# Performance work log

Measured on AMD Instinct MI355X. Metric: run time of the kernel, lower is better.

Reference implementation:

```python
import jax, jax.numpy as jnp
import numpy as np

B, S, D, E, K = 2, 2048, 1024, 8, 2
H = 4 * D  # FFN hidden


def setup_inputs() -> dict:
    key = jax.random.key(0)
    ks = jax.random.split(key, 6)
    x = jax.random.normal(ks[0], (B, S, D), dtype=jnp.float32)
    # xavier-uniform gate
    lim_g = np.sqrt(6.0 / (D + E)).astype(np.float32)
    W_gate = jax.random.uniform(ks[1], (D, E), minval=-lim_g, maxval=lim_g, dtype=jnp.float32)
    # per-expert FFN params, stacked on leading expert axis
    lim1 = np.sqrt(1.0 / D).astype(np.float32)
    lim2 = np.sqrt(1.0 / H).astype(np.float32)
    W1 = jax.random.uniform(ks[2], (E, D, H), minval=-lim1, maxval=lim1, dtype=jnp.float32)
    b1 = jax.random.uniform(ks[3], (E, H), minval=-lim1, maxval=lim1, dtype=jnp.float32)
    W2 = jax.random.uniform(ks[4], (E, H, D), minval=-lim2, maxval=lim2, dtype=jnp.float32)
    b2 = jax.random.uniform(ks[5], (E, D), minval=-lim2, maxval=lim2, dtype=jnp.float32)
    return {"x": x, "W_gate": W_gate, "W1": W1, "b1": b1, "W2": W2, "b2": b2}


def reference(x, W_gate, W1, b1, W2, b2):
    # gating: topk mask then softmax over kept logits
    gate = jnp.einsum('bsd,de->bse', x, W_gate)                      # [B,S,E]
    kth = jax.lax.top_k(gate, K)[0][..., -1:]                        # k-th largest [B,S,1]
    mask = jax.nn.softmax(jnp.where(gate >= kth, gate, -jnp.inf), axis=-1)
    # all-experts FFN (faithful to original dense compute)
    h = jax.nn.relu(jnp.einsum('bsd,edh->bseh', x, W1) + b1)         # [B,S,E,H]
    y = jnp.einsum('bseh,ehd->bsed', h, W2) + b2                     # [B,S,E,D]
    # masked MEAN over experts (original uses .mean, i.e. divides by E)
    return (y * mask[..., None]).mean(axis=-2)                       # [B,S,D]
```

## Files before the change

kernel.cpp:

```cpp
#include <hip/hip_runtime.h>
#include <stdint.h>
#include <stddef.h>

#define TOK   4096
#define DDIM  1024
#define EXP   8
#define HDIM  4096

typedef __bf16 bf16x8 __attribute__((ext_vector_type(8)));
typedef __bf16 bf16x4 __attribute__((ext_vector_type(4)));
typedef __bf16 bf16x2 __attribute__((ext_vector_type(2)));
typedef float  f32x4  __attribute__((ext_vector_type(4)));

#define OFF_COUNTS 0ull
#define OFF_PREFIX 256ull
#define OFF_PERM   512ull
#define OFF_WGT    (OFF_PERM + 131072ull)
#define OFF_XBF    (OFF_WGT + 131072ull)
#define OFF_W1T    (OFF_XBF + 8388608ull)
#define OFF_W2T    (OFF_W1T + 67108864ull)
#define OFF_HBF    (OFF_W2T + 67108864ull)
#define OFF_T2E    (OFF_HBF + 68157440ull)

__device__ __forceinline__ void load16_lds(const void* g, void* l) {
  __builtin_amdgcn_global_load_lds((__attribute__((address_space(1))) void*)g,
                                   (__attribute__((address_space(3))) void*)l,
                                   16, 0, 0);
}

__global__ __launch_bounds__(256) void prep_kernel(
    const float* __restrict__ W1, const float* __restrict__ W2,
    __bf16* __restrict__ W1t, __bf16* __restrict__ W2t,
    const float* __restrict__ x, const float* __restrict__ Wg,
    __bf16* __restrict__ x_bf, int* __restrict__ counts,
    int* __restrict__ perm, float* __restrict__ wgt,
    int4* __restrict__ tok2exp)
{
  __shared__ __align__(16) float tile[2112];
  const int bid = blockIdx.x;
  const int tid = threadIdx.x;

  if (bid < 64) {
    const int lane = tid & 63;
    const int wid  = tid >> 6;

    int*   lcnt   = (int*)tile;
    int*   gbase  = lcnt + 8;
    int*   rec_e  = gbase + 8;
    int*   rec_p  = rec_e + 64;
    float* rec_w0 = (float*)(rec_p + 64);
    float* rec_w1 = rec_w0 + 64;

    if (tid < 8) lcnt[tid] = 0;
    __syncthreads();

#pragma unroll 1
    for (int i = 0; i < 16; ++i) {
      const int li = wid * 16 + i;
      const int t  = bid * 64 + li;
      const float* xr = x + (size_t)t * DDIM;

      float acc[EXP];
#pragma unroll
      for (int e = 0; e < EXP; ++e) acc[e] = 0.f;

#pragma unroll
      for (int it = 0; it < 4; ++it) {
        const int d0 = it * 256 + lane * 4;
        float4 xv = *(const float4*)(xr + d0);
        bf16x4 xb = { (__bf16)xv.x, (__bf16)xv.y, (__bf16)xv.z, (__bf16)xv.w };
        *(bf16x4*)(x_bf + (size_t)t * DDIM + d0) = xb;
        const float* wrow = Wg + (size_t)d0 * EXP;
        float xs[4] = { xv.x, xv.y, xv.z, xv.w };
#pragma unroll
        for (int u = 0; u < 4; ++u) {
          float4 wa = *(const float4*)(wrow + u * 8);
          float4 wb = *(const float4*)(wrow + u * 8 + 4);
          acc[0] += xs[u] * wa.x; acc[1] += xs[u] * wa.y;
          acc[2] += xs[u] * wa.z; acc[3] += xs[u] * wa.w;
          acc[4] += xs[u] * wb.x; acc[5] += xs[u] * wb.y;
          acc[6] += xs[u] * wb.z; acc[7] += xs[u] * wb.w;
        }
      }
#pragma unroll
      for (int e = 0; e < EXP; ++e) {
        float v = acc[e];
#pragma unroll
        for (int s = 32; s > 0; s >>= 1) v += __shfl_down(v, s, 64);
        acc[e] = v;
      }
      if (lane == 0) {
        int e0 = 0; float g0 = acc[0];
#pragma unroll
        for (int e = 1; e < EXP; ++e) if (acc[e] > g0) { g0 = acc[e]; e0 = e; }
        int e1 = 0; float g1 = -3.4e38f;
#pragma unroll
        for (int e = 0; e < EXP; ++e) if (e != e0 && acc[e] > g1) { g1 = acc[e]; e1 = e; }
        float ex = __expf(g1 - g0);
        float m0 = 1.f / (1.f + ex);
        float m1 = ex  / (1.f + ex);
        int lp0 = atomicAdd(&lcnt[e0], 1);
        int lp1 = atomicAdd(&lcnt[e1], 1);
        rec_e[li]  = e0 | (e1 << 8);
        rec_p[li]  = lp0 | (lp1 << 16);
        rec_w0[li] = m0 * 0.125f;
        rec_w1[li] = m1 * 0.125f;
      }
    }
    __syncthreads();
    if (tid < 8) gbase[tid] = atomicAdd(&counts[tid], lcnt[tid]);
    __syncthreads();
    if (tid < 64) {
      const int t = bid * 64 + tid;
      const int ee = rec_e[tid], pp = rec_p[tid];
      const int e0 = ee & 0xff, e1 = ee >> 8;
      const int p0 = gbase[e0] + (pp & 0xffff);
      const int p1 = gbase[e1] + (pp >> 16);
      perm[e0 * TOK + p0] = t;  wgt[e0 * TOK + p0] = rec_w0[tid];
      perm[e1 * TOK + p1] = t;  wgt[e1 * TOK + p1] = rec_w1[tid];
      tok2exp[t] = make_int4(e0, p0, e1, p1);
    }
    return;
  }

  const int tb    = bid - 64;
  const int which = tb >> 13;
  const int e     = (tb >> 10) & 7;
  const int t10   = tb & 1023;
  const float* src; __bf16* dst; int Kd, Nd, tk, tn;
  if (which == 0) { Kd = 1024; Nd = 4096; src = W1; dst = W1t; tk = t10 & 15; tn = t10 >> 4; }
  else            { Kd = 4096; Nd = 1024; src = W2; dst = W2t; tk = t10 >> 4; tn = t10 & 15; }
  const int k0 = tk * 64, n0 = tn * 64;
  src += ((size_t)e * Kd + k0) * Nd + n0;
  dst += ((size_t)e * Nd + n0) * Kd + k0;

  char* tb8 = (char*)tile;
  const int lr2 = (tid >> 4) * 2;
  const int lc  = (tid & 15) * 4;
#pragma unroll
  for (int p = 0; p < 2; ++p) {
    const int r = p * 32 + lr2;
    float4 va = *(const float4*)(src + (size_t)r * Nd + lc);
    float4 vb = *(const float4*)(src + (size_t)(r + 1) * Nd + lc);
    float a4[4] = { va.x, va.y, va.z, va.w };
    float b4[4] = { vb.x, vb.y, vb.z, vb.w };
#pragma unroll
    for (int j = 0; j < 4; ++j) {
      const int n = lc + j;
      bf16x2 w = { (__bf16)a4[j], (__bf16)b4[j] };
      *(bf16x2*)(tb8 + n * 128 + ((r * 2) ^ (((n >> 2) & 7) << 4))) = w;
    }
  }
  __syncthreads();
  const int n2 = tid >> 2, cb = tid & 3;
  const int sw = (n2 >> 2) & 7;
#pragma unroll
  for (int h = 0; h < 2; ++h) {
    const int c = cb + h * 4;
    bf16x8 o = *(const bf16x8*)(tb8 + n2 * 128 + ((c ^ sw) << 4));
    *(bf16x8*)(dst + (size_t)n2 * Kd + c * 8) = o;
  }
}

__global__ __launch_bounds__(256, 2) void gemm1_kernel(
    const __bf16* __restrict__ x_bf, const __bf16* __restrict__ W1t,
    const float* __restrict__ b1, __bf16* __restrict__ h_bf,
    const int* __restrict__ perm, const int* __restrict__ counts)
{
  const int bid = blockIdx.x;
  const int e   = bid >> 10;
  const int mt  = (bid >> 5) & 31;
  const int nt  = bid & 31;
  const int cnt = counts[e];
  if (mt * 128 >= cnt) return;
  int pfx = 0;
#pragma unroll
  for (int i = 0; i < EXP; ++i) if (i < e) pfx += counts[i];

  __shared__ __align__(16) __bf16 As[2][4096];
  __shared__ __align__(16) __bf16 Bs[2][4096];

  const int tid  = threadIdx.x;
  const int lane = tid & 63, wid = tid >> 6;
  const int wm = wid & 1, wn = wid >> 1;
  const int qd = lane >> 4, l15 = lane & 15;

  const int rA0 = tid >> 2, rA1 = rA0 + 64;
  const int pA0 = (tid & 3) ^ ((rA0 >> 1) & 3);
  const int pA1 = (tid & 3) ^ ((rA1 >> 1) & 3);
  int mA0 = mt * 128 + rA0; if (mA0 >= cnt) mA0 = cnt - 1;
  int mA1 = mt * 128 + rA1; if (mA1 >= cnt) mA1 = cnt - 1;
  const int tok0 = perm[e * TOK + mA0];
  const int tok1 = perm[e * TOK + mA1];
  const __bf16* gA0 = x_bf + (size_t)tok0 * DDIM + pA0 * 8;
  const __bf16* gA1 = x_bf + (size_t)tok1 * DDIM + pA1 * 8;
  const __bf16* Wte = W1t + (size_t)e * HDIM * DDIM;
  const __bf16* gB0 = Wte + (size_t)(nt * 128 + rA0) * DDIM + pA0 * 8;
  const __bf16* gB1 = Wte + (size_t)(nt * 128 + rA1) * DDIM + pA1 * 8;

#define STAGE1(buf, kk) do { \
    load16_lds(gA0 + (kk), &As[buf][tid * 8]); \
    load16_lds(gA1 + (kk), &As[buf][(tid + 256) * 8]); \
    load16_lds(gB0 + (kk), &Bs[buf][tid * 8]); \
    load16_lds(gB1 + (kk), &Bs[buf][(tid + 256) * 8]); \
  } while (0)

  f32x4 acc[4][4] = {};

  STAGE1(0, 0);
  __syncthreads();
  int cur = 0;
  for (int kk = 0; kk < DDIM; kk += 32) {
    if (kk + 32 < DDIM) STAGE1(cur ^ 1, kk + 32);
    bf16x8 af[4], bfr[4];
#pragma unroll
    for (int i = 0; i < 4; ++i) {
      int r = wm * 64 + i * 16 + l15;
      int ch = r * 4 + (qd ^ ((r >> 1) & 3));
      af[i] = *(const bf16x8*)(&As[cur][ch * 8]);
    }
#pragma unroll
    for (int j = 0; j < 4; ++j) {
      int r = wn * 64 + j * 16 + l15;
      int ch = r * 4 + (qd ^ ((r >> 1) & 3));
      bfr[j] = *(const bf16x8*)(&Bs[cur][ch * 8]);
    }
#pragma unroll
    for (int i = 0; i < 4; ++i)
#pragma unroll
      for (int j = 0; j < 4; ++j)
        acc[i][j] = __builtin_amdgcn_mfma_f32_16x16x32_bf16(af[i], bfr[j], acc[i][j], 0, 0, 0);
    __syncthreads();
    cur ^= 1;
  }
#undef STAGE1

  const float* b1e = b1 + (size_t)e * HDIM;
#pragma unroll
  for (int i = 0; i < 4; ++i) {
#pragma unroll
    for (int v = 0; v < 4; ++v) {
      const int rl = wm * 64 + i * 16 + qd * 4 + v;
      const int m  = mt * 128 + rl;
      if (m < cnt) {
        __bf16* hrow = h_bf + (size_t)(pfx + m) * HDIM;
#pragma unroll
        for (int j = 0; j < 4; ++j) {
          const int col = nt * 128 + wn * 64 + j * 16 + l15;
          float hv = acc[i][j][v] + b1e[col];
          hv = fmaxf(hv, 0.f);
          hrow[col] = (__bf16)hv;
        }
      }
    }
  }
}

__global__ __launch_bounds__(256, 2) void gemm2_kernel(
    const __bf16* __restrict__ h_bf, const __bf16* __restrict__ W2t,
    __bf16* __restrict__ Y,
    const int* __restrict__ counts)
{
  const int bid = blockIdx.x;
  const int ks  = bid & 3;
  const int nt  = (bid >> 2) & 7;
  const int mt  = (bid >> 5) & 31;
  const int e   = bid >> 10;
  const int cnt = counts[e];
  if (mt * 128 >= cnt) return;
  int pfx = 0;
#pragma unroll
  for (int i = 0; i < EXP; ++i) if (i < e) pfx += counts[i];

  __shared__ __align__(16) __bf16 As[2][4096];
  __shared__ __align__(16) __bf16 Bs[2][4096];

  const int tid  = threadIdx.x;
  const int lane = tid & 63, wid = tid >> 6;
  const int wm = wid & 1, wn = wid >> 1;
  const int qd = lane >> 4, l15 = lane & 15;

  const int rA0 = tid >> 2, rA1 = rA0 + 64;
  const int pA0 = (tid & 3) ^ ((rA0 >> 1) & 3);
  const int pA1 = (tid & 3) ^ ((rA1 >> 1) & 3);
  const __bf16* gA0 = h_bf + (size_t)(pfx + mt * 128 + rA0) * HDIM + pA0 * 8;
  const __bf16* gA1 = h_bf + (size_t)(pfx + mt * 128 + rA1) * HDIM + pA1 * 8;
  const __bf16* Wte = W2t + (size_t)e * DDIM * HDIM;
  const __bf16* gB0 = Wte + (size_t)(nt * 128 + rA0) * HDIM + pA0 * 8;
  const __bf16* gB1 = Wte + (size_t)(nt * 128 + rA1) * HDIM + pA1 * 8;

#define STAGE2(buf, kk) do { \
    load16_lds(gA0 + (kk), &As[buf][tid * 8]); \
    load16_lds(gA1 + (kk), &As[buf][(tid + 256) * 8]); \
    load16_lds(gB0 + (kk), &Bs[buf][tid * 8]); \
    load16_lds(gB1 + (kk), &Bs[buf][(tid + 256) * 8]); \
  } while (0)

  f32x4 acc[4][4] = {};

  const int kbeg = ks * (HDIM / 4);
  const int kend = kbeg + (HDIM / 4);
  STAGE2(0, kbeg);
  __syncthreads();
  int cur = 0;
  for (int kk = kbeg; kk < kend; kk += 32) {
    if (kk + 32 < kend) STAGE2(cur ^ 1, kk + 32);
    bf16x8 af[4], bfr[4];
#pragma unroll
    for (int i = 0; i < 4; ++i) {
      int r = wm * 64 + i * 16 + l15;
      int ch = r * 4 + (qd ^ ((r >> 1) & 3));
      af[i] = *(const bf16x8*)(&As[cur][ch * 8]);
    }
#pragma unroll
    for (int j = 0; j < 4; ++j) {
      int r = wn * 64 + j * 16 + l15;
      int ch = r * 4 + (qd ^ ((r >> 1) & 3));
      bfr[j] = *(const bf16x8*)(&Bs[cur][ch * 8]);
    }
#pragma unroll
    for (int i = 0; i < 4; ++i)
#pragma unroll
      for (int j = 0; j < 4; ++j)
        acc[i][j] = __builtin_amdgcn_mfma_f32_16x16x32_bf16(af[i], bfr[j], acc[i][j], 0, 0, 0);
    __syncthreads();
    cur ^= 1;
  }
#undef STAGE2

  __bf16* Ys = Y + (size_t)ks * (2 * TOK) * DDIM;
#pragma unroll
  for (int i = 0; i < 4; ++i) {
#pragma unroll
    for (int v = 0; v < 4; ++v) {
      const int rl = wm * 64 + i * 16 + qd * 4 + v;
      const int m  = mt * 128 + rl;
      if (m < cnt) {
        __bf16* yrow = Ys + (size_t)(pfx + m) * DDIM;
#pragma unroll
        for (int j = 0; j < 4; ++j) {
          const int col = nt * 128 + wn * 64 + j * 16 + l15;
          yrow[col] = (__bf16)acc[i][j][v];
        }
      }
    }
  }
}

__global__ __launch_bounds__(256) void combine_kernel(
    const __bf16* __restrict__ Y, const float* __restrict__ b2,
    const float* __restrict__ wgt, const int4* __restrict__ tok2exp,
    const int* __restrict__ counts, float* __restrict__ out)
{
  const int t = blockIdx.x;
  const int c = threadIdx.x * 4;
  const int4 m = tok2exp[t];
  int base0 = 0, base1 = 0;
#pragma unroll
  for (int i = 0; i < EXP; ++i) {
    int cc = counts[i];
    if (i < m.x) base0 += cc;
    if (i < m.z) base1 += cc;
  }
  const int g0 = base0 + m.y;
  const int g1 = base1 + m.w;
  const float w0 = wgt[m.x * TOK + m.y];
  const float w1 = wgt[m.z * TOK + m.w];
  const size_t slab = (size_t)(2 * TOK) * DDIM;

  float s0x = 0.f, s0y = 0.f, s0z = 0.f, s0w = 0.f;
  float s1x = 0.f, s1y = 0.f, s1z = 0.f, s1w = 0.f;
#pragma unroll
  for (int s = 0; s < 4; ++s) {
    bf16x4 a = *(const bf16x4*)(Y + s * slab + (size_t)g0 * DDIM + c);
    bf16x4 b = *(const bf16x4*)(Y + s * slab + (size_t)g1 * DDIM + c);
    s0x += (float)a[0]; s0y += (float)a[1]; s0z += (float)a[2]; s0w += (float)a[3];
    s1x += (float)b[0]; s1y += (float)b[1]; s1z += (float)b[2]; s1w += (float)b[3];
  }
  float4 be0 = *(const float4*)(b2 + (size_t)m.x * DDIM + c);
  float4 be1 = *(const float4*)(b2 + (size_t)m.z * DDIM + c);
  float4 r;
  r.x = w0 * (s0x + be0.x) + w1 * (s1x + be1.x);
  r.y = w0 * (s0y + be0.y) + w1 * (s1y + be1.y);
  r.z = w0 * (s0z + be0.z) + w1 * (s1z + be1.z);
  r.w = w0 * (s0w + be0.w) + w1 * (s1w + be1.w);
  *(float4*)(out + (size_t)t * DDIM + c) = r;
}

extern "C" void kernel_launch(void* const* d_in, const int* in_sizes, int n_in,
                              void* d_out, int out_size, void* d_ws, size_t ws_size,
                              hipStream_t stream)
{
  const float* x  = (const float*)d_in[0];
  const float* Wg = (const float*)d_in[1];
  const float* W1 = (const float*)d_in[2];
  const float* b1 = (const float*)d_in[3];
  const float* W2 = (const float*)d_in[4];
  const float* b2 = (const float*)d_in[5];
  float* out = (float*)d_out;

  char* ws = (char*)d_ws;
  int*    counts  = (int*)(ws + OFF_COUNTS);
  int*    perm    = (int*)(ws + OFF_PERM);
  float*  wgt     = (float*)(ws + OFF_WGT);
  __bf16* x_bf    = (__bf16*)(ws + OFF_XBF);
  __bf16* W1t     = (__bf16*)(ws + OFF_W1T);
  __bf16* W2t     = (__bf16*)(ws + OFF_W2T);
  __bf16* h_bf    = (__bf16*)(ws + OFF_HBF);
  int4*   tok2exp = (int4*)(ws + OFF_T2E);
  __bf16* Y       = (__bf16*)(ws + OFF_W1T);

  hipMemsetAsync(counts, 0, 256, stream);

  prep_kernel<<<64 + 16384, 256, 0, stream>>>(W1, W2, W1t, W2t,
                                              x, Wg, x_bf, counts, perm, wgt, tok2exp);
  gemm1_kernel<<<EXP * 32 * 32, 256, 0, stream>>>(x_bf, W1t, b1, h_bf, perm, counts);
  gemm2_kernel<<<EXP * 32 * 8 * 4, 256, 0, stream>>>(h_bf, W2t, Y, counts);
  combine_kernel<<<TOK, 256, 0, stream>>>(Y, b2, wgt, tok2exp, counts, out);
}
```

Before: 540.5 us.

## Overlap W2 transpose with GEMM1 and deepen GEMM K-loop to triple buffering

The W2 fp32→bf16 transpose moves out of the prep kernel and into GEMM1. Odd-numbered GEMM1 blocks do transpose tiles while even-numbered blocks do matrix work, so the memory-bound transpose can overlap with MFMA compute. Both GEMMs switch from double to triple-buffered LDS staging. Each iteration now uses one barrier plus an explicit vmcnt wait instead of two barriers, which keeps two loads in flight. In exchange, LDS use per block grows, and the last two iterations issue loads past the end of the K range into adjacent workspace memory; that data is never consumed.

```diff
diff --git a/kernel.cpp b/kernel.cpp
--- a/kernel.cpp
+++ b/kernel.cpp
@@ -28,9 +28,39 @@
                                    16, 0, 0);
 }
 
+__device__ __forceinline__ void transpose_tile64(const float* __restrict__ src,
+                                                 __bf16* __restrict__ dst,
+                                                 int Nd, int Kd, char* tb8, int tid)
+{
+  const int lr2 = (tid >> 4) * 2;
+  const int lc  = (tid & 15) * 4;
+#pragma unroll
+  for (int p = 0; p < 2; ++p) {
+    const int r = p * 32 + lr2;
+    float4 va = *(const float4*)(src + (size_t)r * Nd + lc);
+    float4 vb = *(const float4*)(src + (size_t)(r + 1) * Nd + lc);
+    float a4[4] = { va.x, va.y, va.z, va.w };
+    float b4[4] = { vb.x, vb.y, vb.z, vb.w };
+#pragma unroll
+    for (int j = 0; j < 4; ++j) {
+      const int n = lc + j;
+      bf16x2 w = { (__bf16)a4[j], (__bf16)b4[j] };
+      *(bf16x2*)(tb8 + n * 128 + ((r * 2) ^ (((n >> 2) & 7) << 4))) = w;
+    }
+  }
+  __syncthreads();
+  const int n2 = tid >> 2, cb = tid & 3;
+  const int sw = (n2 >> 2) & 7;
+#pragma unroll
+  for (int h = 0; h < 2; ++h) {
+    const int c = cb + h * 4;
+    bf16x8 o = *(const bf16x8*)(tb8 + n2 * 128 + ((c ^ sw) << 4));
+    *(bf16x8*)(dst + (size_t)n2 * Kd + c * 8) = o;
+  }
+}
+
 __global__ __launch_bounds__(256) void prep_kernel(
-    const float* __restrict__ W1, const float* __restrict__ W2,
-    __bf16* __restrict__ W1t, __bf16* __restrict__ W2t,
+    const float* __restrict__ W1, __bf16* __restrict__ W1t,
     const float* __restrict__ x, const float* __restrict__ Wg,
     __bf16* __restrict__ x_bf, int* __restrict__ counts,
     int* __restrict__ perm, float* __restrict__ wgt,
@@ -123,64 +153,47 @@
     return;
   }
 
-  const int tb    = bid - 64;
-  const int which = tb >> 13;
-  const int e     = (tb >> 10) & 7;
-  const int t10   = tb & 1023;
-  const float* src; __bf16* dst; int Kd, Nd, tk, tn;
-  if (which == 0) { Kd = 1024; Nd = 4096; src = W1; dst = W1t; tk = t10 & 15; tn = t10 >> 4; }
-  else            { Kd = 4096; Nd = 1024; src = W2; dst = W2t; tk = t10 >> 4; tn = t10 & 15; }
-  const int k0 = tk * 64, n0 = tn * 64;
-  src += ((size_t)e * Kd + k0) * Nd + n0;
-  dst += ((size_t)e * Nd + n0) * Kd + k0;
-
-  char* tb8 = (char*)tile;
-  const int lr2 = (tid >> 4) * 2;
-  const int lc  = (tid & 15) * 4;
-#pragma unroll
-  for (int p = 0; p < 2; ++p) {
-    const int r = p * 32 + lr2;
-    float4 va = *(const float4*)(src + (size_t)r * Nd + lc);
-    float4 vb = *(const float4*)(src + (size_t)(r + 1) * Nd + lc);
-    float a4[4] = { va.x, va.y, va.z, va.w };
-    float b4[4] = { vb.x, vb.y, vb.z, vb.w };
-#pragma unroll
-    for (int j = 0; j < 4; ++j) {
-      const int n = lc + j;
-      bf16x2 w = { (__bf16)a4[j], (__bf16)b4[j] };
-      *(bf16x2*)(tb8 + n * 128 + ((r * 2) ^ (((n >> 2) & 7) << 4))) = w;
-    }
-  }
-  __syncthreads();
-  const int n2 = tid >> 2, cb = tid & 3;
-  const int sw = (n2 >> 2) & 7;
-#pragma unroll
-  for (int h = 0; h < 2; ++h) {
-    const int c = cb + h * 4;
-    bf16x8 o = *(const bf16x8*)(tb8 + n2 * 128 + ((c ^ sw) << 4));
-    *(bf16x8*)(dst + (size_t)n2 * Kd + c * 8) = o;
-  }
+  const int tb  = bid - 64;
+  const int e   = tb >> 10;
+  const int t10 = tb & 1023;
+  const int tk = t10 & 15, tn = t10 >> 4;
+  const float* src = W1 + ((size_t)e * 1024 + tk * 64) * 4096 + tn * 64;
+  __bf16*      dst = W1t + ((size_t)e * 4096 + tn * 64) * 1024 + tk * 64;
+  transpose_tile64(src, dst, 4096, 1024, (char*)tile, tid);
 }
 
 __global__ __launch_bounds__(256, 2) void gemm1_kernel(
     const __bf16* __restrict__ x_bf, const __bf16* __restrict__ W1t,
     const float* __restrict__ b1, __bf16* __restrict__ h_bf,
-    const int* __restrict__ perm, const int* __restrict__ counts)
-{
+    const int* __restrict__ perm, const int* __restrict__ counts,
+    const float* __restrict__ W2, __bf16* __restrict__ W2t)
+{
+  __shared__ __align__(16) __bf16 As[3][4096];
+  __shared__ __align__(16) __bf16 Bs[3][4096];
   const int bid = blockIdx.x;
-  const int e   = bid >> 10;
-  const int mt  = (bid >> 5) & 31;
-  const int nt  = bid & 31;
+  const int tid = threadIdx.x;
+
+  if (bid & 1) {
+    const int p   = bid >> 1;
+    const int e   = p >> 10;
+    const int t10 = p & 1023;
+    const int tk = t10 >> 4, tn = t10 & 15;
+    const float* src = W2 + ((size_t)e * 4096 + tk * 64) * 1024 + tn * 64;
+    __bf16*      dst = W2t + ((size_t)e * 1024 + tn * 64) * 4096 + tk * 64;
+    transpose_tile64(src, dst, 1024, 4096, (char*)As, tid);
+    return;
+  }
+
+  const int g   = bid >> 1;
+  const int e   = g >> 10;
+  const int mt  = (g >> 5) & 31;
+  const int nt  = g & 31;
   const int cnt = counts[e];
   if (mt * 128 >= cnt) return;
   int pfx = 0;
 #pragma unroll
   for (int i = 0; i < EXP; ++i) if (i < e) pfx += counts[i];
 
-  __shared__ __align__(16) __bf16 As[2][4096];
-  __shared__ __align__(16) __bf16 Bs[2][4096];
-
-  const int tid  = threadIdx.x;
   const int lane = tid & 63, wid = tid >> 6;
   const int wm = wid & 1, wn = wid >> 1;
   const int qd = lane >> 4, l15 = lane & 15;
@@ -208,10 +221,15 @@
   f32x4 acc[4][4] = {};
 
   STAGE1(0, 0);
-  __syncthreads();
+  STAGE1(1, 32);
   int cur = 0;
-  for (int kk = 0; kk < DDIM; kk += 32) {
-    if (kk + 32 < DDIM) STAGE1(cur ^ 1, kk + 32);
+#pragma unroll 1
+  for (int it = 0; it < 32; ++it) {
+    asm volatile("s_waitcnt vmcnt(4)" ::: "memory");
+    __builtin_amdgcn_s_barrier();
+    __builtin_amdgcn_sched_barrier(0);
+    int nb = cur + 2; if (nb >= 3) nb -= 3;
+    STAGE1(nb, (it + 2) * 32);
     bf16x8 af[4], bfr[4];
 #pragma unroll
     for (int i = 0; i < 4; ++i) {
@@ -230,8 +248,7 @@
 #pragma unroll
       for (int j = 0; j < 4; ++j)
         acc[i][j] = __builtin_amdgcn_mfma_f32_16x16x32_bf16(af[i], bfr[j], acc[i][j], 0, 0, 0);
-    __syncthreads();
-    cur ^= 1;
+    cur += 1; if (cur == 3) cur = 0;
   }
 #undef STAGE1
 
@@ -272,8 +289,8 @@
 #pragma unroll
   for (int i = 0; i < EXP; ++i) if (i < e) pfx += counts[i];
 
-  __shared__ __align__(16) __bf16 As[2][4096];
-  __shared__ __align__(16) __bf16 Bs[2][4096];
+  __shared__ __align__(16) __bf16 As[3][4096];
+  __shared__ __align__(16) __bf16 Bs[3][4096];
 
   const int tid  = threadIdx.x;
   const int lane = tid & 63, wid = tid >> 6;
@@ -299,12 +316,16 @@
   f32x4 acc[4][4] = {};
 
   const int kbeg = ks * (HDIM / 4);
-  const int kend = kbeg + (HDIM / 4);
   STAGE2(0, kbeg);
-  __syncthreads();
+  STAGE2(1, kbeg + 32);
   int cur = 0;
-  for (int kk = kbeg; kk < kend; kk += 32) {
-    if (kk + 32 < kend) STAGE2(cur ^ 1, kk + 32);
+#pragma unroll 1
+  for (int it = 0; it < 32; ++it) {
+    asm volatile("s_waitcnt vmcnt(4)" ::: "memory");
+    __builtin_amdgcn_s_barrier();
+    __builtin_amdgcn_sched_barrier(0);
+    int nb = cur + 2; if (nb >= 3) nb -= 3;
+    STAGE2(nb, kbeg + (it + 2) * 32);
     bf16x8 af[4], bfr[4];
 #pragma unroll
     for (int i = 0; i < 4; ++i) {
@@ -323,8 +344,7 @@
 #pragma unroll
       for (int j = 0; j < 4; ++j)
         acc[i][j] = __builtin_amdgcn_mfma_f32_16x16x32_bf16(af[i], bfr[j], acc[i][j], 0, 0, 0);
-    __syncthreads();
-    cur ^= 1;
+    cur += 1; if (cur == 3) cur = 0;
   }
 #undef STAGE2
 
@@ -412,9 +432,8 @@
 
   hipMemsetAsync(counts, 0, 256, stream);
 
-  prep_kernel<<<64 + 16384, 256, 0, stream>>>(W1, W2, W1t, W2t,
-                                              x, Wg, x_bf, counts, perm, wgt, tok2exp);
-  gemm1_kernel<<<EXP * 32 * 32, 256, 0, stream>>>(x_bf, W1t, b1, h_bf, perm, counts);
+  prep_kernel<<<64 + 8192, 256, 0, stream>>>(W1, W1t, x, Wg, x_bf, counts, perm, wgt, tok2exp);
+  gemm1_kernel<<<2 * EXP * 32 * 32, 256, 0, stream>>>(x_bf, W1t, b1, h_bf, perm, counts, W2, W2t);
   gemm2_kernel<<<EXP * 32 * 8 * 4, 256, 0, stream>>>(h_bf, W2t, Y, counts);
   combine_kernel<<<TOK, 256, 0, stream>>>(Y, b2, wgt, tok2exp, counts, out);
 }
```

After: 599.5 us. 1.11x slower.
